# Kernel optimization log

Hardware: AMD Instinct MI355X
Metric: run time of the kernel (lower is better)

## Reference

```python
import jax, jax.numpy as jnp
import numpy as np

EPS = 1e-5

def _conv3x3(x, w, b):
    # x: (B,C,H,W), w: (O,I,3,3) OIHW, SAME padding, stride 1
    y = jax.lax.conv_general_dilated(x, w, (1, 1), 'SAME',
                                     dimension_numbers=('NCHW', 'OIHW', 'NCHW'))
    return y + b[None, :, None, None]

def _inorm(x):
    # InstanceNorm2d (affine=False, eval-free): per-sample per-channel over HW
    m = jnp.mean(x, axis=(2, 3), keepdims=True)
    v = jnp.var(x, axis=(2, 3), keepdims=True)
    return (x - m) * jax.lax.rsqrt(v + EPS)

def _pac_conv_transpose(x, guide, w, b, stride=2, padding=1, out_pad=1):
    # PacConvTranspose2d (gaussian kernel, not channel-wise, unnormalized):
    # 1) zero-stuff input by stride, pad by (k-1)-padding (+output_padding on the
    #    bottom/right), 2) run a 3x3 conv whose taps are modulated per-pixel by
    #    K_ij = exp(-0.5 * ||g(p+ij) - g(p)||^2) computed from the guidance map.
    # w: (Cin, Cout, k, k)  (torch transposed-conv layout)
    k = w.shape[2]
    B, C, H, Wd = x.shape
    xs = jnp.zeros((B, C, (H - 1) * stride + 1, (Wd - 1) * stride + 1), x.dtype)
    xs = xs.at[:, :, ::stride, ::stride].set(x)
    p = (k - 1) - padding
    xp = jnp.pad(xs, ((0, 0), (0, 0), (p, p + out_pad), (p, p + out_pad)))
    gpad = (k - 1) // 2
    gp = jnp.pad(guide, ((0, 0), (0, 0), (gpad, gpad), (gpad, gpad)))
    Ho, Wo = guide.shape[2], guide.shape[3]
    out = jnp.zeros((B, w.shape[1], Ho, Wo), x.dtype)
    for i in range(k):          # fixed 3x3 tap loop (not a data-dim loop)
        for j in range(k):
            gn = gp[:, :, i:i + Ho, j:j + Wo]
            kk = jnp.exp(-0.5 * jnp.sum((gn - guide) ** 2, axis=1, keepdims=True))  # (B,1,Ho,Wo)
            xn = xp[:, :, i:i + Ho, j:j + Wo]                                        # (B,Cin,Ho,Wo)
            out = out + jnp.einsum('bchw,co->bohw', xn * kk, w[:, :, i, j])
    return out + b[None, :, None, None]

def setup_inputs() -> dict:
    key = jax.random.key(0)
    ks = jax.random.split(key, 16)
    C = 64
    s = 0.02  # small weight scale to keep gaussian adaptive kernels well-conditioned
    inp = {
        'x':      jax.random.normal(ks[0], (1, 4 * C, 64, 64), jnp.float32),
        'ef_lv2': jax.random.normal(ks[1], (1, 2 * C, 128, 128), jnp.float32),
        'ef_lv1': jax.random.normal(ks[2], (1, C, 256, 256), jnp.float32),
        'w_adj2': jax.random.normal(ks[3], (4 * C, 2 * C, 3, 3), jnp.float32) * s,
        'b_adj2': jnp.zeros((4 * C,), jnp.float32),
        'w_adj1': jax.random.normal(ks[4], (2 * C, C, 3, 3), jnp.float32) * s,
        'b_adj1': jnp.zeros((2 * C,), jnp.float32),
        'w_pac16': jax.random.normal(ks[5], (4 * C, 2 * C, 3, 3), jnp.float32) * s,
        'b_pac16': jnp.zeros((2 * C,), jnp.float32),
        'w_pac20': jax.random.normal(ks[6], (2 * C, C, 3, 3), jnp.float32) * s,
        'b_pac20': jnp.zeros((C,), jnp.float32),
        'w_out':  jax.random.normal(ks[7], (3, C, 3, 3), jnp.float32) * s,
        'b_out':  jnp.zeros((3,), jnp.float32),
    }
    return inp

def reference(x, ef_lv2, ef_lv1, w_adj2, b_adj2, w_adj1, b_adj1,
              w_pac16, b_pac16, w_pac20, b_pac20, w_out, b_out):
    x = _inorm(x) + x                       # layer13 + residual
    x = _inorm(x) + x                       # layer14 + residual
    g2 = _conv3x3(ef_lv2, w_adj2, b_adj2)   # adjust_ef_lv2_pacconv
    x = _pac_conv_transpose(x, g2, w_pac16, b_pac16)  # layer16: 64->128
    x = _inorm(x) + x                       # layer17
    x = _inorm(x) + x                       # layer18
    g1 = _conv3x3(ef_lv1, w_adj1, b_adj1)   # adjust_ef_lv1_pacconv
    x = _pac_conv_transpose(x, g1, w_pac20, b_pac20)  # layer20: 128->256
    x = _inorm(x) + x                       # layer21
    x = _inorm(x) + x                       # layer22
    return _conv3x3(x, w_out, b_out)        # layer24 -> (B,3,256,256)
```

## Files before the change

kernel.cpp:

```cpp
#include <hip/hip_runtime.h>
#include <hip/hip_bf16.h>
#include <cstdint>
#include <cstddef>

#define EPS_IN 1e-5f

typedef __attribute__((ext_vector_type(8))) short short8;
typedef __attribute__((ext_vector_type(4))) float floatx4;
typedef __attribute__((ext_vector_type(8))) unsigned short ushort8;
typedef __attribute__((ext_vector_type(4))) unsigned short ushort4v;
typedef __attribute__((ext_vector_type(4))) unsigned int uint4v;
typedef __attribute__((address_space(3))) unsigned int lds_uint;
typedef __attribute__((address_space(1))) const unsigned int glb_uint;

__device__ __forceinline__ unsigned short f2bf(float f) {
    unsigned int u = __float_as_uint(f);
    u += 0x7FFFu + ((u >> 16) & 1u);
    return (unsigned short)(u >> 16);
}
__device__ __forceinline__ float bf2f(unsigned short s) {
    return __uint_as_float((unsigned int)s << 16);
}
__device__ __forceinline__ float bflo(unsigned int u) {
    return __uint_as_float(u << 16);
}
__device__ __forceinline__ float bfhi(unsigned int u) {
    return __uint_as_float(u & 0xFFFF0000u);
}

__device__ __forceinline__ void composed_norm(float s, float q, float HW,
                                              float& A, float& B) {
    float m1 = s / HW;
    float v1 = q / HW - m1 * m1;
    float r1 = rsqrtf(v1 + EPS_IN);
    float a1 = 1.f + r1;
    float b1 = -m1 * r1;
    float r2 = rsqrtf(a1 * a1 * v1 + EPS_IN);
    float a2 = 1.f + r2;
    A = a1 * a2;
    B = a2 * b1 - m1 * r2;
}

__device__ __forceinline__ void border_zero(unsigned short* buf, int C, int H, int W, int idx) {
    int Hp = H + 2, Wp = W + 2;
    int cg8 = C >> 3;
    int cg = idx % cg8;
    int bi = idx / cg8;
    int y, x;
    if (bi < Wp) { y = 0; x = bi; }
    else if (bi < 2 * Wp) { y = Hp - 1; x = bi - Wp; }
    else {
        int k = bi - 2 * Wp;
        y = 1 + (k >> 1);
        x = (k & 1) ? (Wp - 1) : 0;
    }
    ushort8 z = {0, 0, 0, 0, 0, 0, 0, 0};
    *(ushort8*)&buf[((size_t)y * Wp + x) * C + cg * 8] = z;
}

__device__ __forceinline__ void reorder_one(const float* w, unsigned short* dst,
                                            int O, int C, int j) {
    int cg8 = C >> 3;
    int cg = j % cg8;
    int o = (j / cg8) % O;
    int tap = j / (cg8 * O);
    ushort8 v;
#pragma unroll
    for (int i = 0; i < 8; i++)
        v[i] = f2bf(w[((size_t)o * C + cg * 8 + i) * 9 + tap]);
    *(ushort8*)&dst[((size_t)tap * O + o) * C + cg * 8] = v;
}
__device__ __forceinline__ void stack_one(const float* w, unsigned short* dst,
                                          int C, int O, int j) {
    int cg8 = C >> 3;
    int cg = j % cg8;
    int o = (j / cg8) % O;
    int tap = j / (cg8 * O);
    ushort8 v;
#pragma unroll
    for (int i = 0; i < 8; i++)
        v[i] = f2bf(w[((size_t)(cg * 8 + i) * O + o) * 9 + tap]);
    *(ushort8*)&dst[((size_t)tap * O + o) * C + cg * 8] = v;
}

__device__ __forceinline__ void pad_one(const float* in, unsigned short* xp,
                                        int C, int H, int W, int t) {
    int HW = H * W;
    int p = t % HW;
    int cg = t / HW;
    int y = p / W, x = p % W;
    ushort8 v;
#pragma unroll
    for (int i = 0; i < 8; i++)
        v[i] = f2bf(in[(size_t)(cg * 8 + i) * HW + p]);
    *(ushort8*)&xp[((size_t)(y + 1) * (W + 2) + (x + 1)) * C + cg * 8] = v;
}

__global__ void prologue_kernel(uint4v* __restrict__ statz,
                                unsigned short* __restrict__ xp2,
                                unsigned short* __restrict__ xp1,
                                const float* __restrict__ w_adj2, unsigned short* __restrict__ Wr2,
                                const float* __restrict__ w_adj1, unsigned short* __restrict__ Wr1,
                                const float* __restrict__ w_p16, unsigned short* __restrict__ Wt16,
                                const float* __restrict__ w_p20, unsigned short* __restrict__ Wt20,
                                const float* __restrict__ ef2, const float* __restrict__ ef1,
                                const float* __restrict__ x, float2* __restrict__ statX) {
    __shared__ float ss[4], sq[4];
    int b = blockIdx.x;
    if (b < 68) {
        int t = b * 256 + threadIdx.x;
        const int NZ = 864;
        const int N2 = 516 * 16;
        const int N1 = 1028 * 8;
        if (t < NZ) {
            uint4v z = {0u, 0u, 0u, 0u};
            statz[t] = z;
        } else if (t < NZ + N2) {
            border_zero(xp2, 128, 128, 128, t - NZ);
        } else if (t < NZ + N2 + N1) {
            border_zero(xp1, 64, 256, 256, t - NZ - N2);
        }
    } else if (b < 428) {
        int t = (b - 68) * 256 + threadIdx.x;
        if (t < 36864) reorder_one(w_adj2, Wr2, 256, 128, t);
        else if (t < 46080) reorder_one(w_adj1, Wr1, 128, 64, t - 36864);
        else if (t < 82944) stack_one(w_p16, Wt16, 256, 128, t - 46080);
        else if (t < 92160) stack_one(w_p20, Wt20, 128, 64, t - 82944);
    } else if (b < 3500) {
        int t = (b - 428) * 256 + threadIdx.x;
        if (t < 262144) pad_one(ef2, xp2, 128, 128, 128, t);
        else            pad_one(ef1, xp1, 64, 256, 256, t - 262144);
    } else {
        int c = b - 3500;
        const float* src = x + (size_t)c * 4096;
        float s = 0.f, q = 0.f;
#pragma unroll
        for (int k = 0; k < 4; k++) {
            float4 v = *(const float4*)(src + k * 1024 + threadIdx.x * 4);
            s += v.x + v.y + v.z + v.w;
            q += v.x * v.x + v.y * v.y + v.z * v.z + v.w * v.w;
        }
#pragma unroll
        for (int off = 32; off >= 1; off >>= 1) {
            s += __shfl_down(s, off, 64);
            q += __shfl_down(q, off, 64);
        }
        int wave = threadIdx.x >> 6;
        if ((threadIdx.x & 63) == 0) { ss[wave] = s; sq[wave] = q; }
        __syncthreads();
        if (threadIdx.x == 0) {
            float2 o;
            o.x = ss[0] + ss[1] + ss[2] + ss[3];
            o.y = sq[0] + sq[1] + sq[2] + sq[3];
            statX[c] = o;
        }
    }
}

template <int CIN>
__launch_bounds__(256, 2)
__global__ void conv3x3_mfma_kernel(const unsigned short* __restrict__ xp,
                                    const unsigned short* __restrict__ wre,
                                    const float* __restrict__ bias,
                                    unsigned short* __restrict__ gpl,
                                    int O, int H, int W) {
    __shared__ short Bbuf[390 * 32];
    __shared__ short Abuf[3 * 128 * 32];
    int tid = threadIdx.x;
    int lane = tid & 63, wid = tid >> 6;
    int mi = wid >> 1, ni = wid & 1;
    int l15 = lane & 15, khi = lane >> 4;
    int tpr = W >> 7;
    int y = blockIdx.x / tpr;
    int x0 = (blockIdx.x % tpr) << 7;
    int o0 = blockIdx.y << 7;
    int Wp = W + 2;
    int HW = H * W;

    floatx4 acc[4][4];
#pragma unroll
    for (int sm = 0; sm < 4; sm++)
#pragma unroll
        for (int r = 0; r < 4; r++) {
            float bv = bias[o0 + mi * 64 + sm * 16 + khi * 4 + r];
#pragma unroll
            for (int sn = 0; sn < 4; sn++) acc[sm][sn][r] = bv;
        }

    for (int cc = 0; cc < CIN / 32; cc++) {
        __syncthreads();
#pragma unroll
        for (int k = 0; k < 7; k++) {
            int s = k * 256 + tid;
            if (s < 1560) {
                int r = s >> 2, q = s & 3;
                int dy = r / 130, col = r % 130;
                const unsigned short* g =
                    xp + ((size_t)(y + dy) * Wp + x0 + col) * CIN + cc * 32 + q * 8;
                __builtin_amdgcn_global_load_lds((glb_uint*)g, (lds_uint*)(Bbuf + s * 8), 16, 0, 0);
            }
        }
        for (int dy = 0; dy < 3; dy++) {
            __syncthreads();
#pragma unroll
            for (int k = 0; k < 6; k++) {
                int s = k * 256 + tid;
                int dx = s >> 9, m = (s >> 2) & 127, q = s & 3;
                const unsigned short* g =
                    wre + ((size_t)((dy * 3 + dx) * O + o0 + m)) * CIN + cc * 32 + q * 8;
                __builtin_amdgcn_global_load_lds((glb_uint*)g, (lds_uint*)(Abuf + s * 8), 16, 0, 0);
            }
            __syncthreads();
#pragma unroll
            for (int dx = 0; dx < 3; dx++) {
                short8 a[4], b[4];
#pragma unroll
                for (int sm = 0; sm < 4; sm++)
                    a[sm] = *(const short8*)&Abuf[(dx * 128 + mi * 64 + sm * 16 + l15) * 32 + khi * 8];
#pragma unroll
                for (int sn = 0; sn < 4; sn++)
                    b[sn] = *(const short8*)&Bbuf[(dy * 130 + ni * 64 + sn * 16 + l15 + dx) * 32 + khi * 8];
#pragma unroll
                for (int sm = 0; sm < 4; sm++)
#pragma unroll
                    for (int sn = 0; sn < 4; sn++)
                        acc[sm][sn] = __builtin_amdgcn_mfma_f32_16x16x32_bf16(
                            a[sm], b[sn], acc[sm][sn], 0, 0, 0);
            }
        }
    }
#pragma unroll
    for (int sm = 0; sm < 4; sm++)
#pragma unroll
        for (int sn = 0; sn < 4; sn++) {
            int ob = o0 + mi * 64 + sm * 16 + khi * 4;
            int px = x0 + ni * 64 + sn * 16 + l15;
#pragma unroll
            for (int r = 0; r < 4; r++)
                gpl[(size_t)(ob + r) * HW + (size_t)y * W + px] = f2bf(acc[sm][sn][r]);
        }
}

template <int CIN>
__launch_bounds__(256, 1)
__global__ void conv3x3_mfma_at_kernel(const unsigned short* __restrict__ xp,
                                       const unsigned short* __restrict__ wre,
                                       const float* __restrict__ bias,
                                       unsigned short* __restrict__ gpl,
                                       int O, int H, int W) {
    __shared__ short Bbuf[390 * 32];
    __shared__ short Abuf[9 * 128 * 32];
    int tid = threadIdx.x;
    int lane = tid & 63, wid = tid >> 6;
    int mi = wid >> 1, ni = wid & 1;
    int l15 = lane & 15, khi = lane >> 4;
    int tpr = W >> 7;
    int y = blockIdx.x / tpr;
    int x0 = (blockIdx.x % tpr) << 7;
    int o0 = blockIdx.y << 7;
    int Wp = W + 2;
    int HW = H * W;

    floatx4 acc[4][4];
#pragma unroll
    for (int sm = 0; sm < 4; sm++)
#pragma unroll
        for (int r = 0; r < 4; r++) {
            float bv = bias[o0 + mi * 64 + sm * 16 + khi * 4 + r];
#pragma unroll
            for (int sn = 0; sn < 4; sn++) acc[sm][sn][r] = bv;
        }

    for (int cc = 0; cc < CIN / 32; cc++) {
        __syncthreads();
#pragma unroll
        for (int k = 0; k < 7; k++) {
            int s = k * 256 + tid;
            if (s < 1560) {
                int r = s >> 2, q = s & 3;
                int dy = r / 130, col = r % 130;
                const unsigned short* g =
                    xp + ((size_t)(y + dy) * Wp + x0 + col) * CIN + cc * 32 + q * 8;
                __builtin_amdgcn_global_load_lds((glb_uint*)g, (lds_uint*)(Bbuf + s * 8), 16, 0, 0);
            }
        }
#pragma unroll
        for (int k = 0; k < 18; k++) {
            int s = k * 256 + tid;
            int row = s >> 2, q = s & 3;
            int tap = row >> 7, m = row & 127;
            const unsigned short* g =
                wre + ((size_t)(tap * O + o0 + m)) * CIN + cc * 32 + q * 8;
            __builtin_amdgcn_global_load_lds((glb_uint*)g, (lds_uint*)(Abuf + s * 8), 16, 0, 0);
        }
        __syncthreads();
#pragma unroll
        for (int dy = 0; dy < 3; dy++)
#pragma unroll
            for (int dx = 0; dx < 3; dx++) {
                short8 a[4], b[4];
#pragma unroll
                for (int sm = 0; sm < 4; sm++)
                    a[sm] = *(const short8*)&Abuf[((dy * 3 + dx) * 128 + mi * 64 + sm * 16 + l15) * 32 + khi * 8];
#pragma unroll
                for (int sn = 0; sn < 4; sn++)
                    b[sn] = *(const short8*)&Bbuf[(dy * 130 + ni * 64 + sn * 16 + l15 + dx) * 32 + khi * 8];
#pragma unroll
                for (int sm = 0; sm < 4; sm++)
#pragma unroll
                    for (int sn = 0; sn < 4; sn++)
                        acc[sm][sn] = __builtin_amdgcn_mfma_f32_16x16x32_bf16(
                            a[sm], b[sn], acc[sm][sn], 0, 0, 0);
            }
    }
#pragma unroll
    for (int sm = 0; sm < 4; sm++)
#pragma unroll
        for (int sn = 0; sn < 4; sn++) {
            int ob = o0 + mi * 64 + sm * 16 + khi * 4;
            int px = x0 + ni * 64 + sn * 16 + l15;
#pragma unroll
            for (int r = 0; r < 4; r++)
                gpl[(size_t)(ob + r) * HW + (size_t)y * W + px] = f2bf(acc[sm][sn][r]);
        }
}

template <int CC>
__device__ __forceinline__ void kk_part_body(const unsigned short* __restrict__ g,
                                             float* __restrict__ S,
                                             int H, int W, int c0, int idx) {
    int Wh = W >> 1;
    int y = idx / Wh, xs = idx % Wh;
    int HW = H * W, HW4 = HW >> 2;
    int ys = y >> 1, ry = y & 1;
    bool xg = (xs + 1 < Wh);
    int off2 = xg ? 1 : 0;
    const unsigned short* gy = g + (size_t)y * W + 2 * xs + (size_t)c0 * HW;
    int slot = ys * Wh + xs;

    if (ry == 0) {
        float s3 = 0.f, s5 = 0.f;
        for (int c = 0; c < CC; c++) {
            const unsigned int* p = (const unsigned int*)(gy + (size_t)c * HW);
            unsigned int cc = p[0];
            unsigned int n2 = p[off2];
            float ce = bflo(cc), co = bfhi(cc);
            float d3 = ce - co;
            float d5 = bflo(n2) - co;
            s3 += d3 * d3;
            s5 += d5 * d5;
        }
        S[(size_t)3 * HW4 + slot] = s3;
        S[(size_t)4 * HW4 + slot] = 0.f;
        S[(size_t)5 * HW4 + slot] = xg ? s5 : 0.f;
    } else {
        bool yg = (y + 1 < H);
        float s0 = 0.f, s1 = 0.f, s2 = 0.f, s6 = 0.f, s7 = 0.f, s8 = 0.f;
        if (yg) {
            for (int c = 0; c < CC; c++) {
                const unsigned int* pc = (const unsigned int*)(gy + (size_t)c * HW);
                const unsigned int* pm = (const unsigned int*)(gy - W + (size_t)c * HW);
                const unsigned int* pp = (const unsigned int*)(gy + W + (size_t)c * HW);
                unsigned int cc = pc[0];
                unsigned int m0 = pm[0], m2 = pm[off2];
                unsigned int q0 = pp[0], q2 = pp[off2];
                float ce = bflo(cc), co = bfhi(cc);
                float nm = bflo(m0), np = bflo(q0);
                float d1 = nm - ce, d0 = nm - co, d2 = bflo(m2) - co;
                float d7 = np - ce, d6 = np - co, d8 = bflo(q2) - co;
                s1 += d1 * d1; s0 += d0 * d0; s2 += d2 * d2;
                s7 += d7 * d7; s6 += d6 * d6; s8 += d8 * d8;
            }
        } else {
            for (int c = 0; c < CC; c++) {
                const unsigned int* pc = (const unsigned int*)(gy + (size_t)c * HW);
                const unsigned int* pm = (const unsigned int*)(gy - W + (size_t)c * HW);
                unsigned int cc = pc[0];
                unsigned int m0 = pm[0], m2 = pm[off2];
                float ce = bflo(cc), co = bfhi(cc);
                float nm = bflo(m0);
                float d1 = nm - ce, d0 = nm - co, d2 = bflo(m2) - co;
                s1 += d1 * d1; s0 += d0 * d0; s2 += d2 * d2;
            }
        }
        S[(size_t)0 * HW4 + slot] = s0;
        S[(size_t)1 * HW4 + slot] = s1;
        S[(size_t)2 * HW4 + slot] = xg ? s2 : 0.f;
        S[(size_t)6 * HW4 + slot] = s6;
        S[(size_t)7 * HW4 + slot] = s7;
        S[(size_t)8 * HW4 + slot] = (xg && yg) ? s8 : 0.f;
    }
}

__global__ void kk_merged_kernel(const unsigned short* __restrict__ Gp2, float* __restrict__ Sp2,
                                 const unsigned short* __restrict__ Gp1, float* __restrict__ Sp1) {
    int b = blockIdx.x;
    if (b < 512) {
        int chunk = b >> 5, xblk = b & 31;
        kk_part_body<16>(Gp2, Sp2 + (size_t)chunk * 9 * 4096, 128, 128,
                         chunk * 16, xblk * 256 + (int)threadIdx.x);
    } else {
        b -= 512;
        int chunk = b >> 7, xblk = b & 127;
        kk_part_body<16>(Gp1, Sp1 + (size_t)chunk * 9 * 16384, 256, 256,
                         chunk * 16, xblk * 256 + (int)threadIdx.x);
    }
}

__global__ void reduce_transpose_kernel(const float* __restrict__ Sp2, float* __restrict__ Sf2,
                                        const float* __restrict__ Sp1, float* __restrict__ Sf1,
                                        const float* __restrict__ x,
                                        const float2* __restrict__ statX,
                                        unsigned short* __restrict__ Xt16) {
    int b = blockIdx.x;
    if (b < 144) {
        int i = b * 256 + threadIdx.x;
        if (i < 36864) {
            float s = 0.f;
            for (int ch = 0; ch < 16; ch++) s += Sp2[(size_t)ch * 36864 + i];
            Sf2[i] = s;
        }
    } else if (b < 720) {
        int i = (b - 144) * 256 + threadIdx.x;
        if (i < 147456) {
            float s = 0.f;
            for (int ch = 0; ch < 8; ch++) s += Sp1[(size_t)ch * 147456 + i];
            Sf1[i] = s;
        }
    } else {
        int t = (b - 720) * 256 + threadIdx.x;
        int p = t % 4096;
        int cg = t / 4096;
        float Av[8], Bv[8];
#pragma unroll
        for (int i = 0; i < 8; i++) {
            float2 pp = statX[cg * 8 + i];
            composed_norm(pp.x, pp.y, 4096.f, Av[i], Bv[i]);
        }
        ushort8 v;
#pragma unroll
        for (int i = 0; i < 8; i++) {
            float xv = x[(size_t)(cg * 8 + i) * 4096 + p];
            v[i] = f2bf(fmaf(xv, Av[i], Bv[i]));
        }
        *(ushort8*)&Xt16[(size_t)p * 256 + cg * 8] = v;
    }
}

__global__ void transpose_norm2_bf16_kernel(const unsigned short* __restrict__ in,
                                            const float2* __restrict__ parts, int NB,
                                            unsigned short* __restrict__ xt,
                                            int C, int HW) {
    int t = blockIdx.x * blockDim.x + threadIdx.x;
    int p = t % HW;
    int cg = t / HW;
    float Av[8], Bv[8];
#pragma unroll
    for (int i = 0; i < 8; i++) {
        int c = cg * 8 + i;
        float s = 0.f, q = 0.f;
        for (int nb = 0; nb < NB; nb++) {
            float2 pp = parts[c * NB + nb];
            s += pp.x; q += pp.y;
        }
        composed_norm(s, q, (float)HW, Av[i], Bv[i]);
    }
    ushort8 v;
#pragma unroll
    for (int i = 0; i < 8; i++) {
        float x = bf2f(in[(size_t)(cg * 8 + i) * HW + p]);
        v[i] = f2bf(fmaf(x, Av[i], Bv[i]));
    }
    *(ushort8*)&xt[(size_t)p * C + cg * 8] = v;
}

template <int K>
__launch_bounds__(256, 3)
__global__ void gemm_bt_kernel(const unsigned short* __restrict__ A,
                               const unsigned short* __restrict__ B,
                               unsigned short* __restrict__ P, int N) {
    __shared__ short Ab[128 * 32];
    __shared__ short Bb[128 * 32];
    int tid = threadIdx.x;
    int lane = tid & 63, wid = tid >> 6;
    int mi = wid >> 1, ni = wid & 1;
    int l15 = lane & 15, khi = lane >> 4;
    int m0 = blockIdx.y << 7, n0 = blockIdx.x << 7;

    floatx4 acc[4][4];
#pragma unroll
    for (int sm = 0; sm < 4; sm++)
#pragma unroll
        for (int sn = 0; sn < 4; sn++)
#pragma unroll
            for (int r = 0; r < 4; r++) acc[sm][sn][r] = 0.f;

    for (int kc = 0; kc < K / 32; kc++) {
        __syncthreads();
#pragma unroll
        for (int k = 0; k < 2; k++) {
            int s = k * 256 + tid;
            int row = s >> 2, q = s & 3;
            const unsigned short* ga = A + (size_t)(m0 + row) * K + kc * 32 + q * 8;
            __builtin_amdgcn_global_load_lds((glb_uint*)ga, (lds_uint*)(Ab + s * 8), 16, 0, 0);
            const unsigned short* gb = B + (size_t)(n0 + row) * K + kc * 32 + q * 8;
            __builtin_amdgcn_global_load_lds((glb_uint*)gb, (lds_uint*)(Bb + s * 8), 16, 0, 0);
        }
        __syncthreads();
        short8 a[4], b[4];
#pragma unroll
        for (int sm = 0; sm < 4; sm++)
            a[sm] = *(const short8*)&Ab[(mi * 64 + sm * 16 + l15) * 32 + khi * 8];
#pragma unroll
        for (int sn = 0; sn < 4; sn++)
            b[sn] = *(const short8*)&Bb[(ni * 64 + sn * 16 + l15) * 32 + khi * 8];
#pragma unroll
        for (int sm = 0; sm < 4; sm++)
#pragma unroll
            for (int sn = 0; sn < 4; sn++)
                acc[sm][sn] = __builtin_amdgcn_mfma_f32_16x16x32_bf16(
                    a[sm], b[sn], acc[sm][sn], 0, 0, 0);
    }
#pragma unroll
    for (int sm = 0; sm < 4; sm++)
#pragma unroll
        for (int sn = 0; sn < 4; sn++) {
            int m = m0 + mi * 64 + sm * 16 + khi * 4;
            int n = n0 + ni * 64 + sn * 16 + l15;
#pragma unroll
            for (int r = 0; r < 4; r++)
                P[(size_t)(m + r) * N + n] = f2bf(acc[sm][sn][r]);
        }
}

__global__ void pac_combine2_kernel(const unsigned short* __restrict__ P,
                                    const float* __restrict__ S,
                                    const float* __restrict__ bias,
                                    unsigned short* __restrict__ out,
                                    float2* __restrict__ statOut,
                                    int O, int Hi, int Wi) {
    int HW4 = Hi * Wi;
    int Wo = Wi * 2;
    int HoWo = 4 * HW4;
    int idx = blockIdx.x * blockDim.x + threadIdx.x;
    int pixh = idx % HW4;
    int og = idx / HW4;
    int ys = pixh / Wi, xs = pixh % Wi;
    int ry = blockIdx.z;
    int y = 2 * ys + ry;
    bool xg = (xs + 1 < Wi);
    bool yg = (ys + 1 < Hi);
    size_t rowb = (size_t)ys * Wi + xs;

    float ev[4], ov[4];

    if (ry == 0) {
        float k3 = __expf(-0.5f * S[(size_t)3 * HW4 + pixh]);
        float k4 = __expf(-0.5f * S[(size_t)4 * HW4 + pixh]);
        float k5 = __expf(-0.5f * S[(size_t)5 * HW4 + pixh]);
#pragma unroll
        for (int r = 0; r < 4; r++) {
            int o = og * 4 + r;
            float bv = bias[o];
            const unsigned short* p3 = P + (size_t)(3 * O + o) * HW4 + rowb;
            const unsigned short* p4 = P + (size_t)(4 * O + o) * HW4 + rowb;
            const unsigned short* p5 = P + (size_t)(5 * O + o) * HW4 + rowb;
            float v4 = bf2f(p4[0]);
            float v3 = bf2f(p3[0]);
            float v5 = xg ? bf2f(p5[1]) : 0.f;
            ev[r] = bv + k4 * v4;
            ov[r] = bv + k3 * v3 + k5 * v5;
        }
    } else {
        float k0 = __expf(-0.5f * S[(size_t)0 * HW4 + pixh]);
        float k1 = __expf(-0.5f * S[(size_t)1 * HW4 + pixh]);
        float k2 = __expf(-0.5f * S[(size_t)2 * HW4 + pixh]);
        float k6 = __expf(-0.5f * S[(size_t)6 * HW4 + pixh]);
        float k7 = __expf(-0.5f * S[(size_t)7 * HW4 + pixh]);
        float k8 = __expf(-0.5f * S[(size_t)8 * HW4 + pixh]);
#pragma unroll
        for (int r = 0; r < 4; r++) {
            int o = og * 4 + r;
            float bv = bias[o];
            const unsigned short* p0 = P + (size_t)(0 * O + o) * HW4 + rowb;
            const unsigned short* p1 = P + (size_t)(1 * O + o) * HW4 + rowb;
            const unsigned short* p2 = P + (size_t)(2 * O + o) * HW4 + rowb;
            const unsigned short* p6 = P + (size_t)(6 * O + o) * HW4 + rowb + Wi;
            const unsigned short* p7 = P + (size_t)(7 * O + o) * HW4 + rowb + Wi;
            const unsigned short* p8 = P + (size_t)(8 * O + o) * HW4 + rowb + Wi;
            float v1 = bf2f(p1[0]);
            float v0 = bf2f(p0[0]);
            float v2 = xg ? bf2f(p2[1]) : 0.f;
            float v7 = yg ? bf2f(p7[0]) : 0.f;
            float v6 = yg ? bf2f(p6[0]) : 0.f;
            float v8 = (yg && xg) ? bf2f(p8[1]) : 0.f;
            ev[r] = bv + k1 * v1 + k7 * v7;
            ov[r] = bv + k0 * v0 + k2 * v2 + k6 * v6 + k8 * v8;
        }
    }
#pragma unroll
    for (int r = 0; r < 4; r++) {
        unsigned int pk = (unsigned int)f2bf(ev[r]) | ((unsigned int)f2bf(ov[r]) << 16);
        *(unsigned int*)&out[(size_t)(og * 4 + r) * HoWo + (size_t)y * Wo + 2 * xs] = pk;
    }

    __shared__ float rs[4][4], rq[4][4];
    int wave = threadIdx.x >> 6;
#pragma unroll
    for (int r = 0; r < 4; r++) {
        float s = ev[r] + ov[r];
        float q = ev[r] * ev[r] + ov[r] * ov[r];
#pragma unroll
        for (int off = 32; off >= 1; off >>= 1) {
            s += __shfl_down(s, off, 64);
            q += __shfl_down(q, off, 64);
        }
        if ((threadIdx.x & 63) == 0) { rs[wave][r] = s; rq[wave][r] = q; }
    }
    __syncthreads();
    if (threadIdx.x < 4) {
        int r = threadIdx.x;
        float s = rs[0][r] + rs[1][r] + rs[2][r] + rs[3][r];
        float q = rq[0][r] + rq[1][r] + rq[2][r] + rq[3][r];
        atomicAdd(&statOut[og * 4 + r].x, s);
        atomicAdd(&statOut[og * 4 + r].y, q);
    }
}

__global__ void conv_part_norm_kernel(const unsigned short* __restrict__ in,
                                      const float* __restrict__ w,
                                      const float2* __restrict__ parts, int NB,
                                      float* __restrict__ Pf, int H, int W) {
    __shared__ float wsm[16 * 9 * 3];
    __shared__ float am[16], bm[16];
    int q0 = blockIdx.y * 16;
    int HW = H * W;
    for (int t = threadIdx.x; t < 432; t += blockDim.x) {
        int oc = t % 3;
        int tap = (t / 3) % 9;
        int c = t / 27;
        wsm[t] = w[((size_t)oc * 64 + q0 + c) * 9 + tap];
    }
    if (threadIdx.x < 16) {
        int c = q0 + threadIdx.x;
        float s = 0.f, q = 0.f;
        for (int nb = 0; nb < NB; nb++) {
            float2 pp = parts[c * NB + nb];
            s += pp.x; q += pp.y;
        }
        float A, B;
        composed_norm(s, q, (float)HW, A, B);
        am[threadIdx.x] = A;
        bm[threadIdx.x] = B;
    }
    __syncthreads();
    int pix = blockIdx.x * blockDim.x + threadIdx.x;
    int y = pix / W, x = pix % W;
    float acc[3] = {0.f, 0.f, 0.f};
    bool xl = (x > 0), xr = (x < W - 1);
    for (int c = 0; c < 16; c++) {
        const unsigned short* base = in + (size_t)(q0 + c) * HW + pix;
        const float* wc = wsm + c * 27;
        float ac = am[c], bc = bm[c];
#pragma unroll
        for (int dy = 0; dy < 3; dy++) {
            int yy = y + dy - 1;
            if (yy < 0 || yy >= H) continue;
            const unsigned short* row = base + (dy - 1) * W;
            float v0 = xl ? fmaf(bf2f(row[-1]), ac, bc) : 0.f;
            float v1 = fmaf(bf2f(row[0]), ac, bc);
            float v2 = xr ? fmaf(bf2f(row[1]), ac, bc) : 0.f;
#pragma unroll
            for (int ob = 0; ob < 3; ob++) {
                acc[ob] += v0 * wc[(dy * 3 + 0) * 3 + ob];
                acc[ob] += v1 * wc[(dy * 3 + 1) * 3 + ob];
                acc[ob] += v2 * wc[(dy * 3 + 2) * 3 + ob];
            }
        }
    }
#pragma unroll
    for (int ob = 0; ob < 3; ob++)
        Pf[(size_t)(blockIdx.y * 3 + ob) * HW + pix] = acc[ob];
}

__global__ void conv_fin_kernel(const float* __restrict__ Pf, const float* __restrict__ bias,
                                float* __restrict__ out, int HW) {
    int pix = blockIdx.x * blockDim.x + threadIdx.x;
#pragma unroll
    for (int ob = 0; ob < 3; ob++) {
        float a = bias[ob];
#pragma unroll
        for (int q = 0; q < 4; q++)
            a += Pf[(size_t)(q * 3 + ob) * HW + pix];
        out[(size_t)ob * HW + pix] = a;
    }
}

extern "C" void kernel_launch(void* const* d_in, const int* in_sizes, int n_in,
                              void* d_out, int out_size, void* d_ws, size_t ws_size,
                              hipStream_t stream) {
    const float* x      = (const float*)d_in[0];
    const float* ef2    = (const float*)d_in[1];
    const float* ef1    = (const float*)d_in[2];
    const float* w_adj2 = (const float*)d_in[3];
    const float* b_adj2 = (const float*)d_in[4];
    const float* w_adj1 = (const float*)d_in[5];
    const float* b_adj1 = (const float*)d_in[6];
    const float* w_p16  = (const float*)d_in[7];
    const float* b_p16  = (const float*)d_in[8];
    const float* w_p20  = (const float*)d_in[9];
    const float* b_p20  = (const float*)d_in[10];
    const float* w_out  = (const float*)d_in[11];
    const float* b_out  = (const float*)d_in[12];
    float* out = (float*)d_out;

    float* ws = (float*)d_ws;
    unsigned short* bxb1 = (unsigned short*)(ws + 1048576);
    unsigned short* bxb2 = (unsigned short*)(ws + 3145728);
    unsigned short* Wt16 = (unsigned short*)(ws + 5242880);
    float* bk2c = ws + 7340032;
    float* bk1c = ws + 7376896;
    float2* statX   = (float2*)(ws + 7524352);
    float2* statP16 = (float2*)(ws + 7525376);
    float2* statP20 = (float2*)(ws + 7526656);
    unsigned short* Wt20 = (unsigned short*)(ws + 7528832);
    unsigned short* Gp1  = (unsigned short*)(ws + 7569792);
    unsigned short* P16  = (unsigned short*)(ws + 7569792);
    unsigned short* Xt16 = (unsigned short*)(ws + 9929088);
    unsigned short* P20  = (unsigned short*)(ws + 7569792);
    unsigned short* Gp2  = (unsigned short*)(ws + 12812672);
    unsigned short* Xt20 = (unsigned short*)(ws + 12812672);
    unsigned short* Xp2 = (unsigned short*)(ws + 14975872);
    unsigned short* Wr2 = (unsigned short*)(ws + 16057472);
    unsigned short* Xp1 = (unsigned short*)(ws + 16204928);
    unsigned short* Wr1 = (unsigned short*)(ws + 18334976);
    float* Pf = ws + 14975872;
    float* Sp2 = ws + 18371840;
    float* Sp1 = ws + 18961664;

    prologue_kernel<<<3756, 256, 0, stream>>>(
        (uint4v*)(ws + 7525376), Xp2, Xp1,
        w_adj2, Wr2, w_adj1, Wr1, w_p16, Wt16, w_p20, Wt20,
        ef2, ef1, x, statX);

    conv3x3_mfma_at_kernel<128><<<dim3(128, 2), 256, 0, stream>>>(Xp2, Wr2, b_adj2, Gp2, 256, 128, 128);
    conv3x3_mfma_kernel<64><<<dim3(512, 1), 256, 0, stream>>>(Xp1, Wr1, b_adj1, Gp1, 128, 256, 256);

    kk_merged_kernel<<<1536, 256, 0, stream>>>(Gp2, Sp2, Gp1, Sp1);
    reduce_transpose_kernel<<<1232, 256, 0, stream>>>(Sp2, bk2c, Sp1, bk1c, x, statX, Xt16);

    gemm_bt_kernel<256><<<dim3(32, 9), 256, 0, stream>>>(Wt16, Xt16, P16, 4096);
    pac_combine2_kernel<<<dim3(512, 1, 2), 256, 0, stream>>>(P16, bk2c, b_p16, bxb1, statP16, 128, 64, 64);

    transpose_norm2_bf16_kernel<<<1024, 256, 0, stream>>>(bxb1, statP16, 1, Xt20, 128, 16384);

    gemm_bt_kernel<128><<<dim3(128, 5), 256, 0, stream>>>(Wt20, Xt20, P20, 16384);
    pac_combine2_kernel<<<dim3(1024, 1, 2), 256, 0, stream>>>(P20, bk1c, b_p20, bxb2, statP20, 64, 128, 128);

    conv_part_norm_kernel<<<dim3(256, 4), 256, 0, stream>>>(bxb2, w_out, statP20, 1, Pf, 256, 256);
    conv_fin_kernel<<<256, 256, 0, stream>>>(Pf, b_out, out, 65536);
}
```

Before: 240.3 us.

## Regroup independent stages into merged launches to overlap conv, kk, reduce and GEMM

```diff
diff --git a/kernel.cpp b/kernel.cpp
--- a/kernel.cpp
+++ b/kernel.cpp
@@ -8,7 +8,6 @@
 typedef __attribute__((ext_vector_type(8))) short short8;
 typedef __attribute__((ext_vector_type(4))) float floatx4;
 typedef __attribute__((ext_vector_type(8))) unsigned short ushort8;
-typedef __attribute__((ext_vector_type(4))) unsigned short ushort4v;
 typedef __attribute__((ext_vector_type(4))) unsigned int uint4v;
 typedef __attribute__((address_space(3))) unsigned int lds_uint;
 typedef __attribute__((address_space(1))) const unsigned int glb_uint;
@@ -158,12 +157,11 @@
 }
 
 template <int CIN>
-__launch_bounds__(256, 2)
-__global__ void conv3x3_mfma_kernel(const unsigned short* __restrict__ xp,
-                                    const unsigned short* __restrict__ wre,
-                                    const float* __restrict__ bias,
-                                    unsigned short* __restrict__ gpl,
-                                    int O, int H, int W) {
+__device__ void conv3x3_body(const unsigned short* __restrict__ xp,
+                             const unsigned short* __restrict__ wre,
+                             const float* __restrict__ bias,
+                             unsigned short* __restrict__ gpl,
+                             int O, int H, int W, int bx) {
     __shared__ short Bbuf[390 * 32];
     __shared__ short Abuf[3 * 128 * 32];
     int tid = threadIdx.x;
@@ -171,9 +169,9 @@
     int mi = wid >> 1, ni = wid & 1;
     int l15 = lane & 15, khi = lane >> 4;
     int tpr = W >> 7;
-    int y = blockIdx.x / tpr;
-    int x0 = (blockIdx.x % tpr) << 7;
-    int o0 = blockIdx.y << 7;
+    int y = bx / tpr;
+    int x0 = (bx % tpr) << 7;
+    int o0 = 0;
     int Wp = W + 2;
     int HW = H * W;
 
@@ -392,59 +390,146 @@
     }
 }
 
-__global__ void kk_merged_kernel(const unsigned short* __restrict__ Gp2, float* __restrict__ Sp2,
-                                 const unsigned short* __restrict__ Gp1, float* __restrict__ Sp1) {
+__launch_bounds__(256, 2)
+__global__ void convg1_kk2_kernel(const unsigned short* __restrict__ Xp1,
+                                  const unsigned short* __restrict__ Wr1,
+                                  const float* __restrict__ b_adj1,
+                                  unsigned short* __restrict__ Gp1,
+                                  const unsigned short* __restrict__ Gp2,
+                                  float* __restrict__ Sp2) {
     int b = blockIdx.x;
     if (b < 512) {
+        conv3x3_body<64>(Xp1, Wr1, b_adj1, Gp1, 128, 256, 256, b);
+    } else {
+        b -= 512;
         int chunk = b >> 5, xblk = b & 31;
         kk_part_body<16>(Gp2, Sp2 + (size_t)chunk * 9 * 4096, 128, 128,
                          chunk * 16, xblk * 256 + (int)threadIdx.x);
-    } else {
-        b -= 512;
+    }
+}
+
+__global__ void kk1_red2_transpose_kernel(const unsigned short* __restrict__ Gp1,
+                                          float* __restrict__ Sp1,
+                                          const float* __restrict__ Sp2, float* __restrict__ Sf2,
+                                          const float* __restrict__ x,
+                                          const float2* __restrict__ statX,
+                                          unsigned short* __restrict__ Xt16) {
+    int b = blockIdx.x;
+    if (b < 1024) {
         int chunk = b >> 7, xblk = b & 127;
         kk_part_body<16>(Gp1, Sp1 + (size_t)chunk * 9 * 16384, 256, 256,
                          chunk * 16, xblk * 256 + (int)threadIdx.x);
-    }
-}
-
-__global__ void reduce_transpose_kernel(const float* __restrict__ Sp2, float* __restrict__ Sf2,
-                                        const float* __restrict__ Sp1, float* __restrict__ Sf1,
-                                        const float* __restrict__ x,
-                                        const float2* __restrict__ statX,
-                                        unsigned short* __restrict__ Xt16) {
-    int b = blockIdx.x;
-    if (b < 144) {
-        int i = b * 256 + threadIdx.x;
+    } else if (b < 1168) {
+        int i = (b - 1024) * 256 + threadIdx.x;
         if (i < 36864) {
             float s = 0.f;
             for (int ch = 0; ch < 16; ch++) s += Sp2[(size_t)ch * 36864 + i];
             Sf2[i] = s;
         }
-    } else if (b < 720) {
-        int i = (b - 144) * 256 + threadIdx.x;
+    } else {
+        int t = (b - 1168) * 256 + threadIdx.x;
+        int p = t % 4096;
+        int cg = t / 4096;
+        float Av[8], Bv[8];
+#pragma unroll
+        for (int i = 0; i < 8; i++) {
+            float2 pp = statX[cg * 8 + i];
+            composed_norm(pp.x, pp.y, 4096.f, Av[i], Bv[i]);
+        }
+        ushort8 v;
+#pragma unroll
+        for (int i = 0; i < 8; i++) {
+            float xv = x[(size_t)(cg * 8 + i) * 4096 + p];
+            v[i] = f2bf(fmaf(xv, Av[i], Bv[i]));
+        }
+        *(ushort8*)&Xt16[(size_t)p * 256 + cg * 8] = v;
+    }
+}
+
+template <int K>
+__device__ void gemm_bt_body(const unsigned short* __restrict__ A,
+                             const unsigned short* __restrict__ B,
+                             unsigned short* __restrict__ P, int N,
+                             int m0, int n0) {
+    __shared__ short Ab[128 * 32];
+    __shared__ short Bb[128 * 32];
+    int tid = threadIdx.x;
+    int lane = tid & 63, wid = tid >> 6;
+    int mi = wid >> 1, ni = wid & 1;
+    int l15 = lane & 15, khi = lane >> 4;
+
+    floatx4 acc[4][4];
+#pragma unroll
+    for (int sm = 0; sm < 4; sm++)
+#pragma unroll
+        for (int sn = 0; sn < 4; sn++)
+#pragma unroll
+            for (int r = 0; r < 4; r++) acc[sm][sn][r] = 0.f;
+
+    for (int kc = 0; kc < K / 32; kc++) {
+        __syncthreads();
+#pragma unroll
+        for (int k = 0; k < 2; k++) {
+            int s = k * 256 + tid;
+            int row = s >> 2, q = s & 3;
+            const unsigned short* ga = A + (size_t)(m0 + row) * K + kc * 32 + q * 8;
+            __builtin_amdgcn_global_load_lds((glb_uint*)ga, (lds_uint*)(Ab + s * 8), 16, 0, 0);
+            const unsigned short* gb = B + (size_t)(n0 + row) * K + kc * 32 + q * 8;
+            __builtin_amdgcn_global_load_lds((glb_uint*)gb, (lds_uint*)(Bb + s * 8), 16, 0, 0);
+        }
+        __syncthreads();
+        short8 a[4], b[4];
+#pragma unroll
+        for (int sm = 0; sm < 4; sm++)
+            a[sm] = *(const short8*)&Ab[(mi * 64 + sm * 16 + l15) * 32 + khi * 8];
+#pragma unroll
+        for (int sn = 0; sn < 4; sn++)
+            b[sn] = *(const short8*)&Bb[(ni * 64 + sn * 16 + l15) * 32 + khi * 8];
+#pragma unroll
+        for (int sm = 0; sm < 4; sm++)
+#pragma unroll
+            for (int sn = 0; sn < 4; sn++)
+                acc[sm][sn] = __builtin_amdgcn_mfma_f32_16x16x32_bf16(
+                    a[sm], b[sn], acc[sm][sn], 0, 0, 0);
+    }
+#pragma unroll
+    for (int sm = 0; sm < 4; sm++)
+#pragma unroll
+        for (int sn = 0; sn < 4; sn++) {
+            int m = m0 + mi * 64 + sm * 16 + khi * 4;
+            int n = n0 + ni * 64 + sn * 16 + l15;
+#pragma unroll
+            for (int r = 0; r < 4; r++)
+                P[(size_t)(m + r) * N + n] = f2bf(acc[sm][sn][r]);
+        }
+}
+
+__launch_bounds__(256, 3)
+__global__ void gemm16_red1_kernel(const unsigned short* __restrict__ Wt16,
+                                   const unsigned short* __restrict__ Xt16,
+                                   unsigned short* __restrict__ P16,
+                                   const float* __restrict__ Sp1, float* __restrict__ Sf1) {
+    int b = blockIdx.x;
+    if (b < 288) {
+        int n0 = (b & 31) << 7;
+        int m0 = (b >> 5) << 7;
+        gemm_bt_body<256>(Wt16, Xt16, P16, 4096, m0, n0);
+    } else {
+        int i = (b - 288) * 256 + threadIdx.x;
         if (i < 147456) {
             float s = 0.f;
             for (int ch = 0; ch < 8; ch++) s += Sp1[(size_t)ch * 147456 + i];
             Sf1[i] = s;
         }
-    } else {
-        int t = (b - 720) * 256 + threadIdx.x;
-        int p = t % 4096;
-        int cg = t / 4096;
-        float Av[8], Bv[8];
-#pragma unroll
-        for (int i = 0; i < 8; i++) {
-            float2 pp = statX[cg * 8 + i];
-            composed_norm(pp.x, pp.y, 4096.f, Av[i], Bv[i]);
-        }
-        ushort8 v;
-#pragma unroll
-        for (int i = 0; i < 8; i++) {
-            float xv = x[(size_t)(cg * 8 + i) * 4096 + p];
-            v[i] = f2bf(fmaf(xv, Av[i], Bv[i]));
-        }
-        *(ushort8*)&Xt16[(size_t)p * 256 + cg * 8] = v;
-    }
+    }
+}
+
+template <int K>
+__launch_bounds__(256, 3)
+__global__ void gemm_bt_kernel(const unsigned short* __restrict__ A,
+                               const unsigned short* __restrict__ B,
+                               unsigned short* __restrict__ P, int N) {
+    gemm_bt_body<K>(A, B, P, N, blockIdx.y << 7, blockIdx.x << 7);
 }
 
 __global__ void transpose_norm2_bf16_kernel(const unsigned short* __restrict__ in,
@@ -472,65 +557,6 @@
         v[i] = f2bf(fmaf(x, Av[i], Bv[i]));
     }
     *(ushort8*)&xt[(size_t)p * C + cg * 8] = v;
-}
-
-template <int K>
-__launch_bounds__(256, 3)
-__global__ void gemm_bt_kernel(const unsigned short* __restrict__ A,
-                               const unsigned short* __restrict__ B,
-                               unsigned short* __restrict__ P, int N) {
-    __shared__ short Ab[128 * 32];
-    __shared__ short Bb[128 * 32];
-    int tid = threadIdx.x;
-    int lane = tid & 63, wid = tid >> 6;
-    int mi = wid >> 1, ni = wid & 1;
-    int l15 = lane & 15, khi = lane >> 4;
-    int m0 = blockIdx.y << 7, n0 = blockIdx.x << 7;
-
-    floatx4 acc[4][4];
-#pragma unroll
-    for (int sm = 0; sm < 4; sm++)
-#pragma unroll
-        for (int sn = 0; sn < 4; sn++)
-#pragma unroll
-            for (int r = 0; r < 4; r++) acc[sm][sn][r] = 0.f;
-
-    for (int kc = 0; kc < K / 32; kc++) {
-        __syncthreads();
-#pragma unroll
-        for (int k = 0; k < 2; k++) {
-            int s = k * 256 + tid;
-            int row = s >> 2, q = s & 3;
-            const unsigned short* ga = A + (size_t)(m0 + row) * K + kc * 32 + q * 8;
-            __builtin_amdgcn_global_load_lds((glb_uint*)ga, (lds_uint*)(Ab + s * 8), 16, 0, 0);
-            const unsigned short* gb = B + (size_t)(n0 + row) * K + kc * 32 + q * 8;
-            __builtin_amdgcn_global_load_lds((glb_uint*)gb, (lds_uint*)(Bb + s * 8), 16, 0, 0);
-        }
-        __syncthreads();
-        short8 a[4], b[4];
-#pragma unroll
-        for (int sm = 0; sm < 4; sm++)
-            a[sm] = *(const short8*)&Ab[(mi * 64 + sm * 16 + l15) * 32 + khi * 8];
-#pragma unroll
-        for (int sn = 0; sn < 4; sn++)
-            b[sn] = *(const short8*)&Bb[(ni * 64 + sn * 16 + l15) * 32 + khi * 8];
-#pragma unroll
-        for (int sm = 0; sm < 4; sm++)
-#pragma unroll
-            for (int sn = 0; sn < 4; sn++)
-                acc[sm][sn] = __builtin_amdgcn_mfma_f32_16x16x32_bf16(
-                    a[sm], b[sn], acc[sm][sn], 0, 0, 0);
-    }
-#pragma unroll
-    for (int sm = 0; sm < 4; sm++)
-#pragma unroll
-        for (int sn = 0; sn < 4; sn++) {
-            int m = m0 + mi * 64 + sm * 16 + khi * 4;
-            int n = n0 + ni * 64 + sn * 16 + l15;
-#pragma unroll
-            for (int r = 0; r < 4; r++)
-                P[(size_t)(m + r) * N + n] = f2bf(acc[sm][sn][r]);
-        }
 }
 
 __global__ void pac_combine2_kernel(const unsigned short* __restrict__ P,
@@ -718,6 +744,7 @@
     unsigned short* bxb1 = (unsigned short*)(ws + 1048576);
     unsigned short* bxb2 = (unsigned short*)(ws + 3145728);
     unsigned short* Wt16 = (unsigned short*)(ws + 5242880);
+    unsigned short* Xt16 = (unsigned short*)(ws + 5390336);
     float* bk2c = ws + 7340032;
     float* bk1c = ws + 7376896;
     float2* statX   = (float2*)(ws + 7524352);
@@ -726,7 +753,6 @@
     unsigned short* Wt20 = (unsigned short*)(ws + 7528832);
     unsigned short* Gp1  = (unsigned short*)(ws + 7569792);
     unsigned short* P16  = (unsigned short*)(ws + 7569792);
-    unsigned short* Xt16 = (unsigned short*)(ws + 9929088);
     unsigned short* P20  = (unsigned short*)(ws + 7569792);
     unsigned short* Gp2  = (unsigned short*)(ws + 12812672);
     unsigned short* Xt20 = (unsigned short*)(ws + 12812672);
@@ -744,17 +770,19 @@
         ef2, ef1, x, statX);
 
     conv3x3_mfma_at_kernel<128><<<dim3(128, 2), 256, 0, stream>>>(Xp2, Wr2, b_adj2, Gp2, 256, 128, 128);
-    conv3x3_mfma_kernel<64><<<dim3(512, 1), 256, 0, stream>>>(Xp1, Wr1, b_adj1, Gp1, 128, 256, 256);
-
-    kk_merged_kernel<<<1536, 256, 0, stream>>>(Gp2, Sp2, Gp1, Sp1);
-    reduce_transpose_kernel<<<1232, 256, 0, stream>>>(Sp2, bk2c, Sp1, bk1c, x, statX, Xt16);
-
-    gemm_bt_kernel<256><<<dim3(32, 9), 256, 0, stream>>>(Wt16, Xt16, P16, 4096);
+
+    convg1_kk2_kernel<<<1024, 256, 0, stream>>>(Xp1, Wr1, b_adj1, Gp1, Gp2, Sp2);
+
+    kk1_red2_transpose_kernel<<<1680, 256, 0, stream>>>(Gp1, Sp1, Sp2, bk2c, x, statX, Xt16);
+
+    gemm16_red1_kernel<<<864, 256, 0, stream>>>(Wt16, Xt16, P16, Sp1, bk1c);
+
     pac_combine2_kernel<<<dim3(512, 1, 2), 256, 0, stream>>>(P16, bk2c, b_p16, bxb1, statP16, 128, 64, 64);
 
     transpose_norm2_bf16_kernel<<<1024, 256, 0, stream>>>(bxb1, statP16, 1, Xt20, 128, 16384);
 
     gemm_bt_kernel<128><<<dim3(128, 5), 256, 0, stream>>>(Wt20, Xt20, P20, 16384);
+
     pac_combine2_kernel<<<dim3(1024, 1, 2), 256, 0, stream>>>(P20, bk1c, b_p20, bxb2, statP20, 64, 128, 128);
 
     conv_part_norm_kernel<<<dim3(256, 4), 256, 0, stream>>>(bxb2, w_out, statP20, 1, Pf, 256, 256);
```

Result: faster. 234.1 us (-2.6%).
